# Performance work log

Hardware: AMD Instinct MI355X
Metric: run time of the kernel (lower is better)

The kernel has to match this reference:

```python
import jax, jax.numpy as jnp
import numpy as np

C, H, W = 16, 260, 346   # time bins, sensor height, sensor width (DAVIS346)
N = 16_000_000           # number of events
NUM_VOX = 2 * C * H * W  # B=1, two polarities


def setup_inputs() -> dict:
    key = jax.random.key(0)
    kx, ky, kt, kp = jax.random.split(key, 4)
    x = jax.random.randint(kx, (N,), 0, W).astype(jnp.float32)
    y = jax.random.randint(ky, (N,), 0, H).astype(jnp.float32)
    t = jax.random.uniform(kt, (N,), minval=1e-6, maxval=1.0)
    p = (2 * jax.random.randint(kp, (N,), 0, 2) - 1).astype(jnp.float32)  # {-1, 1}
    events = jnp.stack([x, y, t, p], axis=1)  # [N, 4]
    return {"events": events}


def reference(events):
    x, y, t, p_raw = events.T  # each [N]
    # per-batch t normalization (B=1; batch id read from last column == 0)
    m = p_raw == 0
    tmax = jnp.max(jnp.where(m, t, -jnp.inf))
    t = jnp.where(m & jnp.any(m), t / tmax, t)
    p = (p_raw + 1) * 0.5          # {-1,1} -> {0,1}
    b = 0.0                        # single sample, batch offset 0
    # bin i such that i/C < t <= (i+1)/C  <=>  i = ceil(t*C) - 1
    i_bin = jnp.ceil(t * C) - 1.0
    valid = (t > 0.0) & (t <= 1.0)
    idx = x + W * y + W * H * C * p + W * H * C * 2 * b + W * H * i_bin
    idx = jnp.where(valid, idx, float(NUM_VOX)).astype(jnp.int32)  # sentinel -> dropped
    vox = jnp.zeros((NUM_VOX,), dtype=events.dtype)
    vox = vox.at[idx].set(1.0, mode="drop")  # non-accumulating scatter (put_)
    return vox.reshape(-1, 2, C, H, W)
```

## Files before the change

### kernel.cpp

```cpp
#include <hip/hip_runtime.h>


#define CBINS 16
#define HDIM  260
#define WDIM  346
#define NVOX  (2 * CBINS * HDIM * WDIM)
#define NBUCK 256
#define RGN   11264
#define CHUNK 7424
#define CAP   131072u
#define SENT  0xFFFFFFFFu

typedef float fvec4 __attribute__((ext_vector_type(4)));

__device__ __forceinline__ unsigned ev_to_packed(fvec4 e) {
    float t = e.z;
    if (!(t > 0.f && t <= 1.f)) return SENT;
    int xi  = (int)e.x;
    int yi  = (int)e.y;
    int pi  = (e.w > 0.f) ? 1 : 0;
    int bin = (int)ceilf(t * (float)CBINS) - 1;
    unsigned idx = (unsigned)(xi + WDIM * yi + WDIM * HDIM * (bin + CBINS * pi));
    unsigned b = idx / (unsigned)RGN;
    return (b << 16) | (idx - b * (unsigned)RGN);
}

__global__ __launch_bounds__(256) void partition_kernel(
        const fvec4* __restrict__ ev, int n,
        unsigned short* __restrict__ seg,
        unsigned* __restrict__ gcur) {
    __shared__ unsigned       raw[CHUNK];
    __shared__ unsigned short srt[CHUNK];
    __shared__ unsigned hist[NBUCK + 1];
    __shared__ unsigned scan[NBUCK];
    __shared__ unsigned bnd[NBUCK + 1];
    __shared__ unsigned cursor[NBUCK];
    __shared__ unsigned sbase[NBUCK];

    const int w = blockIdx.x, tid = threadIdx.x;
    const int base = w * CHUNK;
    const int nev = min(CHUNK, n - base);

    for (int b = tid; b <= NBUCK; b += 256) hist[b] = 0;
    __syncthreads();

    int k = tid;
    for (; k + 768 < nev; k += 1024) {
        fvec4 e0 = __builtin_nontemporal_load(&ev[base + k]);
        fvec4 e1 = __builtin_nontemporal_load(&ev[base + k + 256]);
        fvec4 e2 = __builtin_nontemporal_load(&ev[base + k + 512]);
        fvec4 e3 = __builtin_nontemporal_load(&ev[base + k + 768]);
        unsigned i0 = ev_to_packed(e0), i1 = ev_to_packed(e1);
        unsigned i2 = ev_to_packed(e2), i3 = ev_to_packed(e3);
        raw[k]       = i0; raw[k + 256] = i1;
        raw[k + 512] = i2; raw[k + 768] = i3;
        atomicAdd(&hist[(i0 == SENT) ? NBUCK : (i0 >> 16)], 1u);
        atomicAdd(&hist[(i1 == SENT) ? NBUCK : (i1 >> 16)], 1u);
        atomicAdd(&hist[(i2 == SENT) ? NBUCK : (i2 >> 16)], 1u);
        atomicAdd(&hist[(i3 == SENT) ? NBUCK : (i3 >> 16)], 1u);
    }
    for (; k < nev; k += 256) {
        unsigned i0 = ev_to_packed(__builtin_nontemporal_load(&ev[base + k]));
        raw[k] = i0;
        atomicAdd(&hist[(i0 == SENT) ? NBUCK : (i0 >> 16)], 1u);
    }
    __syncthreads();

    unsigned v = hist[tid];
    scan[tid] = v;
    __syncthreads();
    for (int s = 1; s < 256; s <<= 1) {
        unsigned add = (tid >= s) ? scan[tid - s] : 0u;
        __syncthreads();
        scan[tid] += add;
        __syncthreads();
    }
    unsigned excl = scan[tid] - v;
    cursor[tid] = excl;
    bnd[tid] = excl;
    if (tid == 255) bnd[256] = scan[255];
    sbase[tid] = atomicAdd(&gcur[tid], v);
    __syncthreads();

    for (k = tid; k < nev; k += 256) {
        unsigned vv = raw[k];
        if (vv != SENT) {
            unsigned pos = atomicAdd(&cursor[vv >> 16], 1u);
            srt[pos] = (unsigned short)(vv & 0xFFFFu);
        }
    }
    __syncthreads();

    const int wave = tid >> 6, lane = tid & 63;
    for (int b = wave * 64; b < wave * 64 + 64; ++b) {
        unsigned s = bnd[b], e = bnd[b + 1];
        unsigned gb = sbase[b];
        unsigned short* dst = seg + (size_t)b * CAP;
        for (unsigned j = lane; j < e - s; j += 64) {
            unsigned d = gb + j;
            if (d < CAP) dst[d] = srt[s + j];
        }
    }
}

__global__ __launch_bounds__(1024) void build_kernel(
        const unsigned short* __restrict__ seg,
        const unsigned* __restrict__ gcur,
        fvec4* __restrict__ out) {
    __shared__ unsigned char flag[RGN];
    const int b = blockIdx.x, tid = threadIdx.x;

    for (int i = tid; i < RGN / 4; i += 1024) ((unsigned*)flag)[i] = 0;
    __syncthreads();

    unsigned n_b = min(gcur[b], CAP);
    const unsigned* p32 = (const unsigned*)(seg + (size_t)b * CAP);
    for (unsigned j = tid; j < n_b / 2; j += 1024) {
        unsigned v = __builtin_nontemporal_load(&p32[j]);
        flag[v & 0xFFFFu] = 1;
        flag[v >> 16]     = 1;
    }
    if (tid == 0 && (n_b & 1))
        flag[(seg + (size_t)b * CAP)[n_b - 1]] = 1;
    __syncthreads();

    for (int i = tid; i < RGN / 4; i += 1024) {
        int g = b * (RGN / 4) + i;
        if (g < NVOX / 4) {
            uchar4 f = ((const uchar4*)flag)[i];
            fvec4 vv = { f.x ? 1.f : 0.f, f.y ? 1.f : 0.f,
                         f.z ? 1.f : 0.f, f.w ? 1.f : 0.f };
            __builtin_nontemporal_store(vv, &out[g]);
        }
    }
}

__global__ __launch_bounds__(256) void scatter_flags(const fvec4* __restrict__ ev,
                                                     unsigned char* __restrict__ flags,
                                                     int n) {
    int i = blockIdx.x * blockDim.x + threadIdx.x;
    if (i >= n) return;
    fvec4 e = __builtin_nontemporal_load(&ev[i]);
    float t = e.z;
    if (t > 0.f && t <= 1.f) {
        int xi = (int)e.x, yi = (int)e.y;
        int pi = (e.w > 0.f) ? 1 : 0;
        int bin = (int)ceilf(t * (float)CBINS) - 1;
        flags[xi + WDIM * yi + WDIM * HDIM * (bin + CBINS * pi)] = 1;
    }
}
__global__ __launch_bounds__(256) void expand_flags(const uchar4* __restrict__ flags,
                                                    fvec4* __restrict__ out, int n4) {
    int i = blockIdx.x * blockDim.x + threadIdx.x;
    if (i >= n4) return;
    uchar4 f = flags[i];
    fvec4 v = { f.x ? 1.f : 0.f, f.y ? 1.f : 0.f, f.z ? 1.f : 0.f, f.w ? 1.f : 0.f };
    __builtin_nontemporal_store(v, &out[i]);
}

extern "C" void kernel_launch(void* const* d_in, const int* in_sizes, int n_in,
                              void* d_out, int out_size, void* d_ws, size_t ws_size,
                              hipStream_t stream) {
    const fvec4* ev = (const fvec4*)d_in[0];
    int n  = in_sizes[0] / 4;
    int n4 = out_size / 4;
    int nchunk = (n + CHUNK - 1) / CHUNK;

    size_t seg_bytes = (size_t)NBUCK * CAP * sizeof(unsigned short);
    size_t cur_bytes = NBUCK * sizeof(unsigned);

    if (ws_size >= seg_bytes + cur_bytes) {
        unsigned short* seg = (unsigned short*)d_ws;
        unsigned* gcur = (unsigned*)((char*)d_ws + seg_bytes);
        hipMemsetAsync(gcur, 0, cur_bytes, stream);
        partition_kernel<<<nchunk, 256, 0, stream>>>(ev, n, seg, gcur);
        build_kernel<<<NBUCK, 1024, 0, stream>>>(seg, gcur, (fvec4*)d_out);
    } else {
        unsigned char* flags = (unsigned char*)d_ws;
        hipMemsetAsync(flags, 0, NVOX, stream);
        scatter_flags<<<(n + 255) / 256, 256, 0, stream>>>(ev, flags, n);
        expand_flags<<<(n4 + 255) / 256, 256, 0, stream>>>((const uchar4*)flags,
                                                           (fvec4*)d_out, n4);
    }
}
```

Before: 393.2 us.

## Use per-wave histograms, shuffle scan, padded segment writes and FMA indexing

The partition kernel now keeps one shared-memory histogram per wave, which cuts contention on the bucket atomics. The 256-entry scan, which was a barrier-heavy loop, is replaced by a wave shuffle scan plus a small cross-wave fixup. Each block's per-bucket segment is padded to a multiple of 32 and filled with an out-of-range sentinel. That aligns the global stores and lets the build kernel drop its odd-length tail handling, at the cost of extra segment traffic and a larger shared flag array. Voxel index computation moves to float FMAs, and the CAP bounds check on segment writes is removed, which risks overflow if a bucket's padded count exceeds capacity.

```diff
diff --git a/kernel.cpp b/kernel.cpp
--- a/kernel.cpp
+++ b/kernel.cpp
@@ -16,11 +16,11 @@
 __device__ __forceinline__ unsigned ev_to_packed(fvec4 e) {
     float t = e.z;
     if (!(t > 0.f && t <= 1.f)) return SENT;
-    int xi  = (int)e.x;
-    int yi  = (int)e.y;
-    int pi  = (e.w > 0.f) ? 1 : 0;
-    int bin = (int)ceilf(t * (float)CBINS) - 1;
-    unsigned idx = (unsigned)(xi + WDIM * yi + WDIM * HDIM * (bin + CBINS * pi));
+    float bin = __builtin_ceilf(t * 16.f) - 1.f;
+    float bp  = (e.w > 0.f) ? (bin + 16.f) : bin;
+    float idxf = __builtin_fmaf(346.f, e.y, e.x);
+    idxf = __builtin_fmaf(89960.f, bp, idxf);
+    unsigned idx = (unsigned)idxf;
     unsigned b = idx / (unsigned)RGN;
     return (b << 16) | (idx - b * (unsigned)RGN);
 }
@@ -31,19 +31,24 @@
         unsigned* __restrict__ gcur) {
     __shared__ unsigned       raw[CHUNK];
     __shared__ unsigned short srt[CHUNK];
-    __shared__ unsigned hist[NBUCK + 1];
-    __shared__ unsigned scan[NBUCK];
-    __shared__ unsigned bnd[NBUCK + 1];
+    __shared__ unsigned hist4[4][NBUCK];
+    __shared__ unsigned bnd[NBUCK];
+    __shared__ unsigned lenA[NBUCK];
     __shared__ unsigned cursor[NBUCK];
     __shared__ unsigned sbase[NBUCK];
+    __shared__ unsigned wsum[4];
 
     const int w = blockIdx.x, tid = threadIdx.x;
+    const int wave = tid >> 6, lane = tid & 63;
     const int base = w * CHUNK;
     const int nev = min(CHUNK, n - base);
 
-    for (int b = tid; b <= NBUCK; b += 256) hist[b] = 0;
+    hist4[0][tid >> 2 | ((tid & 3) << 6)] = 0;
+    hist4[1][tid] = 0; hist4[2][tid] = 0; hist4[3][tid] = 0;
+    hist4[0][tid] = 0;
     __syncthreads();
 
+    unsigned* myh = hist4[wave];
     int k = tid;
     for (; k + 768 < nev; k += 1024) {
         fvec4 e0 = __builtin_nontemporal_load(&ev[base + k]);
@@ -54,32 +59,36 @@
         unsigned i2 = ev_to_packed(e2), i3 = ev_to_packed(e3);
         raw[k]       = i0; raw[k + 256] = i1;
         raw[k + 512] = i2; raw[k + 768] = i3;
-        atomicAdd(&hist[(i0 == SENT) ? NBUCK : (i0 >> 16)], 1u);
-        atomicAdd(&hist[(i1 == SENT) ? NBUCK : (i1 >> 16)], 1u);
-        atomicAdd(&hist[(i2 == SENT) ? NBUCK : (i2 >> 16)], 1u);
-        atomicAdd(&hist[(i3 == SENT) ? NBUCK : (i3 >> 16)], 1u);
+        if (i0 != SENT) atomicAdd(&myh[i0 >> 16], 1u);
+        if (i1 != SENT) atomicAdd(&myh[i1 >> 16], 1u);
+        if (i2 != SENT) atomicAdd(&myh[i2 >> 16], 1u);
+        if (i3 != SENT) atomicAdd(&myh[i3 >> 16], 1u);
     }
     for (; k < nev; k += 256) {
         unsigned i0 = ev_to_packed(__builtin_nontemporal_load(&ev[base + k]));
         raw[k] = i0;
-        atomicAdd(&hist[(i0 == SENT) ? NBUCK : (i0 >> 16)], 1u);
+        if (i0 != SENT) atomicAdd(&myh[i0 >> 16], 1u);
     }
     __syncthreads();
 
-    unsigned v = hist[tid];
-    scan[tid] = v;
+    unsigned val = hist4[0][tid] + hist4[1][tid] + hist4[2][tid] + hist4[3][tid];
+    unsigned incl = val;
+    #pragma unroll
+    for (int s = 1; s < 64; s <<= 1) {
+        unsigned u = __shfl_up(incl, s, 64);
+        if (lane >= s) incl += u;
+    }
+    if (lane == 63) wsum[wave] = incl;
     __syncthreads();
-    for (int s = 1; s < 256; s <<= 1) {
-        unsigned add = (tid >= s) ? scan[tid - s] : 0u;
-        __syncthreads();
-        scan[tid] += add;
-        __syncthreads();
-    }
-    unsigned excl = scan[tid] - v;
+    unsigned off = 0;
+    if (wave > 0) off += wsum[0];
+    if (wave > 1) off += wsum[1];
+    if (wave > 2) off += wsum[2];
+    unsigned excl = incl - val + off;
+    bnd[tid]  = excl;
+    lenA[tid] = val;
     cursor[tid] = excl;
-    bnd[tid] = excl;
-    if (tid == 255) bnd[256] = scan[255];
-    sbase[tid] = atomicAdd(&gcur[tid], v);
+    sbase[tid] = atomicAdd(&gcur[tid], (val + 31u) & ~31u);
     __syncthreads();
 
     for (k = tid; k < nev; k += 256) {
@@ -91,15 +100,13 @@
     }
     __syncthreads();
 
-    const int wave = tid >> 6, lane = tid & 63;
-    for (int b = wave * 64; b < wave * 64 + 64; ++b) {
-        unsigned s = bnd[b], e = bnd[b + 1];
-        unsigned gb = sbase[b];
-        unsigned short* dst = seg + (size_t)b * CAP;
-        for (unsigned j = lane; j < e - s; j += 64) {
-            unsigned d = gb + j;
-            if (d < CAP) dst[d] = srt[s + j];
-        }
+    for (int b = wave; b < NBUCK; b += 4) {
+        unsigned s   = bnd[b], len = lenA[b];
+        unsigned gb  = sbase[b];
+        unsigned plen = (len + 31u) & ~31u;
+        unsigned short* dst = seg + (size_t)b * CAP + gb;
+        for (unsigned j = lane; j < plen; j += 64)
+            dst[j] = (j < len) ? srt[s + j] : (unsigned short)RGN;
     }
 }
 
@@ -107,10 +114,10 @@
         const unsigned short* __restrict__ seg,
         const unsigned* __restrict__ gcur,
         fvec4* __restrict__ out) {
-    __shared__ unsigned char flag[RGN];
+    __shared__ unsigned char flag[12288];
     const int b = blockIdx.x, tid = threadIdx.x;
 
-    for (int i = tid; i < RGN / 4; i += 1024) ((unsigned*)flag)[i] = 0;
+    for (int i = tid; i < 12288 / 4; i += 1024) ((unsigned*)flag)[i] = 0;
     __syncthreads();
 
     unsigned n_b = min(gcur[b], CAP);
@@ -120,8 +127,6 @@
         flag[v & 0xFFFFu] = 1;
         flag[v >> 16]     = 1;
     }
-    if (tid == 0 && (n_b & 1))
-        flag[(seg + (size_t)b * CAP)[n_b - 1]] = 1;
     __syncthreads();
 
     for (int i = tid; i < RGN / 4; i += 1024) {
```

New measurement: 388.4 us. About the same (-1.2%).
